# Optimization experiments

Measured on AMD Instinct MI355X. Metric: run time of the kernel, lower is better.

The kernel has to match this reference:

```python
import jax, jax.numpy as jnp
import numpy as np

B, C, HH, WW = 4, 128, 64, 64
NH = 2                      # n_heads
D = C // NH                 # head dim
N = HH * WW                 # tokens


def setup_inputs() -> dict:
    key = jax.random.key(0)
    ks = jax.random.split(key, 8)
    s = 1.0 / np.sqrt(C)
    return {
        "x": jax.random.normal(ks[0], (B, C, HH, WW), dtype=jnp.float32),
        "wq": jax.random.normal(ks[1], (C, C), dtype=jnp.float32) * s,
        "bq": jnp.zeros((C,), dtype=jnp.float32),
        "wk": jax.random.normal(ks[2], (C, C), dtype=jnp.float32) * s,
        "bk": jnp.zeros((C,), dtype=jnp.float32),
        "wv": jax.random.normal(ks[3], (C, C), dtype=jnp.float32) * s,
        "bv": jnp.zeros((C,), dtype=jnp.float32),
        "pe": jax.random.normal(ks[4], (N, D, NH), dtype=jnp.float32),
    }


def reference(x, wq, bq, wk, bk, wv, bv, pe):
    b, c, h, w = x.shape
    nh = pe.shape[2]
    d = c // nh
    n = h * w
    xf = x.reshape(b, c, n)                       # flatten spatial -> tokens
    # 1x1 convs == per-pixel channel matmuls
    q = jnp.einsum('oc,bcn->bon', wq, xf) + bq[None, :, None]
    k = jnp.einsum('oc,bcn->bon', wk, xf) + bk[None, :, None]
    v = jnp.einsum('oc,bcn->bon', wv, xf) + bv[None, :, None]
    q = q.reshape(b, nh, d, n)
    k = k.reshape(b, nh, d, n)
    v = v.reshape(b, nh, d, n)
    # learned positional encoding added to q: pe [n, d, nh] -> [nh, d, n]
    q = q + jnp.transpose(pe, (2, 1, 0))[None]
    scale = jnp.asarray(c, x.dtype) ** -0.25
    scores = jnp.einsum('bhdn,bhdm->bhnm', q, k) * scale   # [b,nh,n,n]
    attn = jax.nn.softmax(scores, axis=-1)
    # dropout is identity in eval mode
    o = jnp.einsum('bhnm,bhdm->bhdn', attn, v)             # [b,nh,d,n]
    attn_out = jnp.transpose(o.reshape(b, nh, d, h, w), (0, 2, 1, 3, 4))
    out = attn_out.reshape(b, c, h, w)
    return (out, attn_out)
```

## Files before the change

kernel.cpp:

```cpp
#include <hip/hip_runtime.h>
#include <hip/hip_bf16.h>

typedef unsigned short ushort_t;
typedef unsigned int   uint_t;
typedef unsigned short ushortx8 __attribute__((ext_vector_type(8)));
typedef unsigned short ushortx4 __attribute__((ext_vector_type(4)));
typedef unsigned int   uintx4   __attribute__((ext_vector_type(4)));
typedef __bf16        bf16x8   __attribute__((ext_vector_type(8)));
typedef float         f32x4    __attribute__((ext_vector_type(4)));
typedef float         f32x16   __attribute__((ext_vector_type(16)));

#define SCALE_QL (0.29730177875068026f * 1.4426950408889634f)
#define OUT_HALF 2097152
#define NSPLIT   4
#define KT_SPLIT 16
#define MFIX     32.0f

static __device__ __forceinline__ float fexp2(float x) {
    float r; asm("v_exp_f32 %0, %1" : "=v"(r) : "v"(x)); return r;
}
static __device__ __forceinline__ unsigned cvtpk_bf16(float lo, float hi) {
    unsigned r;
    asm("v_cvt_pk_bf16_f32 %0, %1, %2" : "=v"(r) : "v"(lo), "v"(hi));
    return r;
}
static __device__ __forceinline__ void pswap(unsigned& a, unsigned& b) {
    asm("v_permlane32_swap_b32 %0, %1" : "+v"(a), "+v"(b));
}
static __device__ __forceinline__ ushort_t bf16u(float f) {
    __hip_bfloat16 h = __float2bfloat16(f);
    return __builtin_bit_cast(ushort_t, h);
}
static __device__ __forceinline__ float bflo(unsigned u) {
    return __builtin_bit_cast(float, u << 16);
}
static __device__ __forceinline__ float bfhi(unsigned u) {
    return __builtin_bit_cast(float, u & 0xffff0000u);
}
static __device__ __forceinline__ void glds16(const void* g, void* l) {
    __builtin_amdgcn_global_load_lds(
        (const __attribute__((address_space(1))) unsigned int*)g,
        (__attribute__((address_space(3))) unsigned int*)l, 16, 0, 0);
}

__global__ __launch_bounds__(256) void prep_kernel(
    const float* __restrict__ pe,
    const float* __restrict__ wq, const float* __restrict__ wk,
    const float* __restrict__ wv,
    float* __restrict__ pet, ushort_t* __restrict__ wb)
{
    const int bid = blockIdx.x, t = threadIdx.x;
    if (bid < 1024) {
        int idx = bid * 256 + t;
        float2 p2 = *(const float2*)(pe + (size_t)idx * 2);
        pet[idx]                     = p2.x;
        pet[(size_t)4096 * 64 + idx] = p2.y;
        return;
    }
    const int b2 = bid - 1024;
    const int p  = b2 >> 3;
    const float* w = (p == 0) ? wq : (p == 1) ? wk : wv;
    const int cid = (b2 & 7) * 256 + t;
    const int o = cid >> 4, chunk = cid & 15;
    float4 f0 = *(const float4*)(w + o * 128 + chunk * 8);
    float4 f1 = *(const float4*)(w + o * 128 + chunk * 8 + 4);
    ushortx8 u;
    u[0] = bf16u(f0.x); u[1] = bf16u(f0.y); u[2] = bf16u(f0.z); u[3] = bf16u(f0.w);
    u[4] = bf16u(f1.x); u[5] = bf16u(f1.y); u[6] = bf16u(f1.z); u[7] = bf16u(f1.w);
    *(ushortx8*)(wb + p * 16384 + o * 128 + ((chunk ^ (o & 15)) << 3)) = u;
}

__global__ __launch_bounds__(256, 2) void proj_kernel(
    const float* __restrict__ x, const ushort_t* __restrict__ wb,
    const float* __restrict__ bq, const float* __restrict__ bk,
    const float* __restrict__ bv, const float* __restrict__ pet,
    ushort_t* __restrict__ qw, ushort_t* __restrict__ kw,
    ushort_t* __restrict__ vw)
{
    const int ntl = blockIdx.x;
    const int b = blockIdx.y;
    __shared__ __align__(16) ushort_t xt[64 * 128];
    __shared__ __align__(16) union {
        ushort_t xs[128][68];
        ushort_t wt[16384];
    } smu;
    const int t = threadIdx.x, lane = t & 63;
    const int wv_ = __builtin_amdgcn_readfirstlane(t >> 6);
    const int l16 = lane & 15, lhi = lane >> 4;

    {
        const int cg = t >> 4, n0 = (t & 15) * 4;
#pragma unroll
        for (int i = 0; i < 8; ++i) {
            int c = i * 16 + cg;
            float4 f = *(const float4*)(x + ((size_t)(b * 128 + c)) * 4096 + ntl * 64 + n0);
            ushortx4 u;
            u[0] = bf16u(f.x); u[1] = bf16u(f.y); u[2] = bf16u(f.z); u[3] = bf16u(f.w);
            *(ushortx4*)(&smu.xs[c][n0]) = u;
        }
    }
    __syncthreads();
    {
        const int n = t >> 2;
#pragma unroll
        for (int j = 0; j < 4; ++j) {
            int chunk = (t & 3) * 4 + j;
            ushortx8 u;
#pragma unroll
            for (int e = 0; e < 8; ++e) u[e] = smu.xs[chunk * 8 + e][n];
            *(ushortx8*)(xt + n * 128 + ((chunk ^ (n & 15)) << 3)) = u;
        }
    }

    const int nbase = ntl * 64;
    const char* xbp = (const char*)xt;
    const char* wbp = (const char*)smu.wt;

    for (int p = 0; p < 3; ++p) {
        __syncthreads();
        const ushort_t* wsrc = wb + p * 16384;
#pragma unroll
        for (int j = 0; j < 8; ++j) {
            int row = wv_ * 32 + j * 4;
            glds16(wsrc + row * 128 + lane * 8, smu.wt + row * 128);
        }

        const float* bias = (p == 0) ? bq : (p == 1) ? bk : bv;
        f32x4 bias4[2];
        bias4[0] = *(const f32x4*)(bias + wv_ * 32 + lhi * 4);
        bias4[1] = *(const f32x4*)(bias + wv_ * 32 + 16 + lhi * 4);
        f32x4 acc[2][4];
#pragma unroll
        for (int mf = 0; mf < 2; ++mf)
#pragma unroll
            for (int nf = 0; nf < 4; ++nf) acc[mf][nf] = bias4[mf];

        __syncthreads();

#pragma unroll
        for (int ks = 0; ks < 4; ++ks) {
            bf16x8 af[2];
#pragma unroll
            for (int mf = 0; mf < 2; ++mf) {
                int row = wv_ * 32 + mf * 16 + l16;
                af[mf] = __builtin_bit_cast(bf16x8, *(const ushortx8*)(
                    wbp + row * 256 + ((((ks * 4 + lhi) ^ l16) & 15) << 4)));
            }
#pragma unroll
            for (int nf = 0; nf < 4; ++nf) {
                int row = nf * 16 + l16;
                bf16x8 bfr = __builtin_bit_cast(bf16x8, *(const ushortx8*)(
                    xbp + row * 256 + ((((ks * 4 + lhi) ^ l16) & 15) << 4)));
                acc[0][nf] = __builtin_amdgcn_mfma_f32_16x16x32_bf16(af[0], bfr, acc[0][nf], 0, 0, 0);
                acc[1][nf] = __builtin_amdgcn_mfma_f32_16x16x32_bf16(af[1], bfr, acc[1][nf], 0, 0, 0);
            }
        }

        if (p == 2) {
#pragma unroll
            for (int mf = 0; mf < 2; ++mf) {
                int o = wv_ * 32 + mf * 16 + lhi * 4;
                int h = o >> 6, d = o & 63;
                ushort_t* vb = vw + (((size_t)(b * 2 + h) * 64 + d)) * 4096 + nbase + l16;
#pragma unroll
                for (int nf = 0; nf < 4; ++nf)
#pragma unroll
                    for (int r = 0; r < 4; ++r)
                        vb[(size_t)r * 4096 + nf * 16] = bf16u(acc[mf][nf][r]);
            }
        } else if (p == 0) {
#pragma unroll
            for (int mf = 0; mf < 2; ++mf) {
                int o = wv_ * 32 + mf * 16 + lhi * 4;
                int h = o >> 6, d = o & 63;
#pragma unroll
                for (int nf = 0; nf < 4; ++nf) {
                    int n = nbase + nf * 16 + l16;
                    f32x4 pe4 = *(const f32x4*)(pet + ((size_t)h * 4096 + n) * 64 + d);
                    f32x4 q4 = (acc[mf][nf] + pe4) * SCALE_QL;
                    ushortx4 s;
                    s[0] = bf16u(q4[0]); s[1] = bf16u(q4[1]);
                    s[2] = bf16u(q4[2]); s[3] = bf16u(q4[3]);
                    *(ushortx4*)(qw + ((size_t)(b * 2 + h) * 4096 + n) * 64 + d) = s;
                }
            }
        } else {
#pragma unroll
            for (int mf = 0; mf < 2; ++mf) {
                int o = wv_ * 32 + mf * 16 + lhi * 4;
                int h = o >> 6, d = o & 63;
#pragma unroll
                for (int nf = 0; nf < 4; ++nf) {
                    int n = nbase + nf * 16 + l16;
                    f32x4 k4 = acc[mf][nf];
                    ushortx4 s;
                    s[0] = bf16u(k4[0]); s[1] = bf16u(k4[1]);
                    s[2] = bf16u(k4[2]); s[3] = bf16u(k4[3]);
                    *(ushortx4*)(kw + ((size_t)(b * 2 + h) * 4096 + n) * 64 + d) = s;
                }
            }
        }
    }
}

__global__ __launch_bounds__(512, 4) void attn_kernel(
    const ushort_t* __restrict__ qw, const ushort_t* __restrict__ kw,
    const ushort_t* __restrict__ vw, uint_t* __restrict__ opart,
    float* __restrict__ lspart)
{
    const int qt = blockIdx.x, bh = blockIdx.y, sp = blockIdx.z;
    const int t = threadIdx.x, lane = t & 63;
    const int wv = t >> 6;
    const int l31 = lane & 31, hi = lane >> 5;

    __shared__ __align__(16) ushort_t Kt[2 * 64 * 64];
    __shared__ __align__(16) ushort_t Vt[2 * 64 * 64];

    const int qb = qt * 256 + wv * 32;
    bf16x8 qf[4];
#pragma unroll
    for (int ks = 0; ks < 4; ++ks)
        qf[ks] = __builtin_bit_cast(bf16x8, *(const ushortx8*)(
            qw + ((size_t)bh * 4096 + qb + l31) * 64 + ks * 16 + hi * 8));

    const ushort_t* kgb = kw + ((size_t)bh * 4096) * 64;
    const ushort_t* vgb = vw + ((size_t)bh * 64) * 4096;

    const int srow = lane >> 3, c7 = lane & 7;
    const int rb = wv * 8;
    const int swz = (c7 ^ srow) << 3;
    const size_t koff = (size_t)(rb + srow) * 64 + swz;
    const size_t voff = (size_t)(rb + srow) * 4096 + swz;

    const f32x16 z16 = {0,0,0,0,0,0,0,0,0,0,0,0,0,0,0,0};
    f32x16 oa0 = z16, oa1 = z16;
    float ls0 = 0.f;

    const int kt0 = sp * KT_SPLIT;

#define STAGE(buf, ktb)                                                       \
    {                                                                         \
        glds16(kgb + (size_t)(ktb) * 4096 + koff,                             \
               Kt + (buf) * 4096 + (size_t)rb * 64);                          \
        glds16(vgb + (size_t)(ktb) * 64 + voff,                               \
               Vt + (buf) * 4096 + (size_t)rb * 64);                          \
    }

    STAGE(0, kt0)
    __syncthreads();

    const int sw7 = l31 & 7;
    int cur = 0;
    for (int it = 0; it < KT_SPLIT; ++it) {
        const int itn = (it + 1 < KT_SPLIT) ? it + 1 : it;
        STAGE(cur ^ 1, kt0 + itn)

        const char* kc = (const char*)(Kt + cur * 4096);
        const char* vc = (const char*)(Vt + cur * 4096);

#pragma unroll
        for (int c = 0; c < 2; ++c) {
            const int kbase = (c * 32 + l31) * 128;
            bf16x8 kf[4];
#pragma unroll
            for (int ks = 0; ks < 4; ++ks)
                kf[ks] = __builtin_bit_cast(bf16x8, *(const ushortx8*)(
                    kc + kbase + (((ks * 2 + hi) ^ sw7) << 4)));

            f32x16 s0 = z16;
            __builtin_amdgcn_s_setprio(1);
#pragma unroll
            for (int ks = 0; ks < 4; ++ks)
                s0 = __builtin_amdgcn_mfma_f32_32x32x16_bf16(kf[ks], qf[ks], s0, 0, 0, 0);
            __builtin_amdgcn_s_setprio(0);

            float p[16];
#pragma unroll
            for (int r = 0; r < 16; ++r) p[r] = fexp2(s0[r] - MFIX);
            float q0 = (p[0] + p[1]) + (p[2] + p[3]);
            float q1 = (p[4] + p[5]) + (p[6] + p[7]);
            float q2 = (p[8] + p[9]) + (p[10] + p[11]);
            float q3 = (p[12] + p[13]) + (p[14] + p[15]);
            ls0 += (q0 + q1) + (q2 + q3);
            unsigned c0 = cvtpk_bf16(p[0], p[1]);
            unsigned c1 = cvtpk_bf16(p[2], p[3]);
            unsigned c2 = cvtpk_bf16(p[4], p[5]);
            unsigned c3 = cvtpk_bf16(p[6], p[7]);
            unsigned c4 = cvtpk_bf16(p[8], p[9]);
            unsigned c5 = cvtpk_bf16(p[10], p[11]);
            unsigned c6 = cvtpk_bf16(p[12], p[13]);
            unsigned c7x = cvtpk_bf16(p[14], p[15]);
            pswap(c0, c2); pswap(c1, c3); pswap(c4, c6); pswap(c5, c7x);
            bf16x8 pfa, pfb;
            { uintx4 u; u[0] = c0; u[1] = c1; u[2] = c2; u[3] = c3;
              pfa = __builtin_bit_cast(bf16x8, u); }
            { uintx4 u; u[0] = c4; u[1] = c5; u[2] = c6; u[3] = c7x;
              pfb = __builtin_bit_cast(bf16x8, u); }

            __builtin_amdgcn_s_setprio(1);
            {
                const int vb0 = l31 * 128;
                bf16x8 vf0 = __builtin_bit_cast(bf16x8, *(const ushortx8*)(
                    vc + vb0 + ((((c * 2 + 0) * 2 + hi) ^ sw7) << 4)));
                bf16x8 vf1 = __builtin_bit_cast(bf16x8, *(const ushortx8*)(
                    vc + vb0 + ((((c * 2 + 1) * 2 + hi) ^ sw7) << 4)));
                oa0 = __builtin_amdgcn_mfma_f32_32x32x16_bf16(vf0, pfa, oa0, 0, 0, 0);
                oa0 = __builtin_amdgcn_mfma_f32_32x32x16_bf16(vf1, pfb, oa0, 0, 0, 0);
            }
            {
                const int vb1 = (32 + l31) * 128;
                bf16x8 vf0 = __builtin_bit_cast(bf16x8, *(const ushortx8*)(
                    vc + vb1 + ((((c * 2 + 0) * 2 + hi) ^ sw7) << 4)));
                bf16x8 vf1 = __builtin_bit_cast(bf16x8, *(const ushortx8*)(
                    vc + vb1 + ((((c * 2 + 1) * 2 + hi) ^ sw7) << 4)));
                oa1 = __builtin_amdgcn_mfma_f32_32x32x16_bf16(vf0, pfa, oa1, 0, 0, 0);
                oa1 = __builtin_amdgcn_mfma_f32_32x32x16_bf16(vf1, pfb, oa1, 0, 0, 0);
            }
            __builtin_amdgcn_s_setprio(0);
        }

        __syncthreads();
        cur ^= 1;
    }

    const int pidx = (qt * 8 + bh) * NSPLIT + sp;
#define STORE_OA(OA, DT)                                                      \
    {                                                                         \
        uintx4 u0, u1;                                                        \
        u0[0] = cvtpk_bf16(OA[0], OA[1]);  u0[1] = cvtpk_bf16(OA[2], OA[3]);  \
        u0[2] = cvtpk_bf16(OA[4], OA[5]);  u0[3] = cvtpk_bf16(OA[6], OA[7]);  \
        u1[0] = cvtpk_bf16(OA[8], OA[9]);  u1[1] = cvtpk_bf16(OA[10], OA[11]);\
        u1[2] = cvtpk_bf16(OA[12], OA[13]);u1[3] = cvtpk_bf16(OA[14], OA[15]);\
        uint_t* dst = opart +                                                 \
            (((size_t)pidx * 8 + wv) * 2 + (DT)) * 512 + lane * 8;            \
        *(uintx4*)dst = u0; *(uintx4*)(dst + 4) = u1;                         \
    }
    STORE_OA(oa0, 0) STORE_OA(oa1, 1)

    ls0 += __shfl_xor(ls0, 32, 64);
    if (hi == 0)
        lspart[(pidx * 8 + wv) * 32 + l31] = ls0;
}

__global__ __launch_bounds__(512) void combine_kernel(
    const uint_t* __restrict__ opart, const float* __restrict__ lspart,
    float* __restrict__ out)
{
    const int qt = blockIdx.x, bh = blockIdx.y;
    const int b = bh >> 1, h = bh & 1;
    const int t = threadIdx.x, lane = t & 63, wa = t >> 6;
    const int l31 = lane & 31, hi = lane >> 5;
    const int pbase = (qt * 8 + bh) * NSPLIT;
    const int dtbl[8] = {0, 2, 8, 10, 16, 18, 24, 26};

    float den = 0.f;
#pragma unroll
    for (int sp = 0; sp < NSPLIT; ++sp)
        den += lspart[((pbase + sp) * 8 + wa) * 32 + l31];
    float inv = 1.f / den;

    const int q = qt * 256 + wa * 32 + l31;
#pragma unroll
    for (int dt = 0; dt < 2; ++dt) {
        float acc[16];
#pragma unroll
        for (int i = 0; i < 16; ++i) acc[i] = 0.f;
#pragma unroll
        for (int sp = 0; sp < NSPLIT; ++sp) {
            const uint_t* src = opart +
                (((size_t)(pbase + sp) * 8 + wa) * 2 + dt) * 512 + lane * 8;
            uintx4 a = *(const uintx4*)src;
            uintx4 b2 = *(const uintx4*)(src + 4);
#pragma unroll
            for (int j = 0; j < 4; ++j) {
                acc[2 * j]     += bflo(a[j]);
                acc[2 * j + 1] += bfhi(a[j]);
                acc[8 + 2 * j] += bflo(b2[j]);
                acc[9 + 2 * j] += bfhi(b2[j]);
            }
        }
#pragma unroll
        for (int j = 0; j < 8; ++j) {
            int d = dt * 32 + 4 * hi + dtbl[j];
            float v0 = acc[2 * j] * inv;
            float v1 = acc[2 * j + 1] * inv;
            size_t o0 = ((size_t)(b * 128 + d * 2 + h)) * 4096 + q;
            out[o0] = v0;
            out[o0 + OUT_HALF] = v0;
            size_t o1 = o0 + 2 * 4096;
            out[o1] = v1;
            out[o1 + OUT_HALF] = v1;
        }
    }
}

extern "C" void kernel_launch(void* const* d_in, const int* in_sizes, int n_in,
                              void* d_out, int out_size, void* d_ws, size_t ws_size,
                              hipStream_t stream) {
    const float* x  = (const float*)d_in[0];
    const float* wq = (const float*)d_in[1];
    const float* bq = (const float*)d_in[2];
    const float* wk = (const float*)d_in[3];
    const float* bk = (const float*)d_in[4];
    const float* wv = (const float*)d_in[5];
    const float* bv = (const float*)d_in[6];
    const float* pe = (const float*)d_in[7];
    float* out = (float*)d_out;

    char* ws = (char*)d_ws;
    float*    pet   = (float*)ws;
    ushort_t* qw    = (ushort_t*)(ws + (size_t)2  * 1024 * 1024);
    ushort_t* kw    = (ushort_t*)(ws + (size_t)6  * 1024 * 1024);
    ushort_t* vw    = (ushort_t*)(ws + (size_t)10 * 1024 * 1024);
    uint_t*   opart = (uint_t*)(ws + (size_t)14 * 1024 * 1024);
    float*    lsprt = (float*)(ws + (size_t)31 * 1024 * 1024);
    ushort_t* wb    = (ushort_t*)(ws + (size_t)31 * 1024 * 1024);

    hipLaunchKernelGGL(prep_kernel, dim3(1048), dim3(256), 0, stream,
                       pe, wq, wk, wv, pet, wb);
    hipLaunchKernelGGL(proj_kernel, dim3(64, 4), dim3(256), 0, stream,
                       x, wb, bq, bk, bv, pet, qw, kw, vw);
    hipLaunchKernelGGL(attn_kernel, dim3(16, 8, NSPLIT), dim3(512), 0, stream,
                       qw, kw, vw, opart, lsprt);
    hipLaunchKernelGGL(combine_kernel, dim3(16, 8), dim3(512), 0, stream,
                       opart, lsprt, out);
}
```

Baseline: 70.53 us.

## Split projection across grid z and double attention K/V tile size

The projection kernel now launches one block per (tile, batch, projection) instead of looping over Q/K/V in one block. This triples the block count to improve occupancy, but each block reloads and converts the x tile. The attention kernel stages 128-key tiles instead of 64 and halves the per-split iteration count, which cuts barriers and loop overhead per key. In exchange it doubles LDS use for the K/V double buffers, which may reduce how many blocks fit on a CU.

```diff
diff --git a/kernel.cpp b/kernel.cpp
--- a/kernel.cpp
+++ b/kernel.cpp
@@ -13,7 +13,7 @@
 #define SCALE_QL (0.29730177875068026f * 1.4426950408889634f)
 #define OUT_HALF 2097152
 #define NSPLIT   4
-#define KT_SPLIT 16
+#define KT_SPLIT 8
 #define MFIX     32.0f
 
 static __device__ __forceinline__ float fexp2(float x) {
@@ -78,7 +78,7 @@
     ushort_t* __restrict__ vw)
 {
     const int ntl = blockIdx.x;
-    const int b = blockIdx.y;
+    const int b = blockIdx.y, p = blockIdx.z;
     __shared__ __align__(16) ushort_t xt[64 * 128];
     __shared__ __align__(16) union {
         ushort_t xs[128][68];
@@ -111,93 +111,92 @@
             *(ushortx8*)(xt + n * 128 + ((chunk ^ (n & 15)) << 3)) = u;
         }
     }
+    __syncthreads();
+
+    {
+        const ushort_t* wsrc = wb + p * 16384;
+#pragma unroll
+        for (int j = 0; j < 8; ++j) {
+            int row = wv_ * 32 + j * 4;
+            glds16(wsrc + row * 128 + lane * 8, smu.wt + row * 128);
+        }
+    }
+
+    const float* bias = (p == 0) ? bq : (p == 1) ? bk : bv;
+    f32x4 bias4[2];
+    bias4[0] = *(const f32x4*)(bias + wv_ * 32 + lhi * 4);
+    bias4[1] = *(const f32x4*)(bias + wv_ * 32 + 16 + lhi * 4);
+    f32x4 acc[2][4];
+#pragma unroll
+    for (int mf = 0; mf < 2; ++mf)
+#pragma unroll
+        for (int nf = 0; nf < 4; ++nf) acc[mf][nf] = bias4[mf];
+
+    __syncthreads();
 
     const int nbase = ntl * 64;
     const char* xbp = (const char*)xt;
     const char* wbp = (const char*)smu.wt;
-
-    for (int p = 0; p < 3; ++p) {
-        __syncthreads();
-        const ushort_t* wsrc = wb + p * 16384;
-#pragma unroll
-        for (int j = 0; j < 8; ++j) {
-            int row = wv_ * 32 + j * 4;
-            glds16(wsrc + row * 128 + lane * 8, smu.wt + row * 128);
-        }
-
-        const float* bias = (p == 0) ? bq : (p == 1) ? bk : bv;
-        f32x4 bias4[2];
-        bias4[0] = *(const f32x4*)(bias + wv_ * 32 + lhi * 4);
-        bias4[1] = *(const f32x4*)(bias + wv_ * 32 + 16 + lhi * 4);
-        f32x4 acc[2][4];
-#pragma unroll
-        for (int mf = 0; mf < 2; ++mf)
-#pragma unroll
-            for (int nf = 0; nf < 4; ++nf) acc[mf][nf] = bias4[mf];
-
-        __syncthreads();
-
-#pragma unroll
-        for (int ks = 0; ks < 4; ++ks) {
-            bf16x8 af[2];
-#pragma unroll
-            for (int mf = 0; mf < 2; ++mf) {
-                int row = wv_ * 32 + mf * 16 + l16;
-                af[mf] = __builtin_bit_cast(bf16x8, *(const ushortx8*)(
-                    wbp + row * 256 + ((((ks * 4 + lhi) ^ l16) & 15) << 4)));
+#pragma unroll
+    for (int ks = 0; ks < 4; ++ks) {
+        bf16x8 af[2];
+#pragma unroll
+        for (int mf = 0; mf < 2; ++mf) {
+            int row = wv_ * 32 + mf * 16 + l16;
+            af[mf] = __builtin_bit_cast(bf16x8, *(const ushortx8*)(
+                wbp + row * 256 + ((((ks * 4 + lhi) ^ l16) & 15) << 4)));
+        }
+#pragma unroll
+        for (int nf = 0; nf < 4; ++nf) {
+            int row = nf * 16 + l16;
+            bf16x8 bfr = __builtin_bit_cast(bf16x8, *(const ushortx8*)(
+                xbp + row * 256 + ((((ks * 4 + lhi) ^ l16) & 15) << 4)));
+            acc[0][nf] = __builtin_amdgcn_mfma_f32_16x16x32_bf16(af[0], bfr, acc[0][nf], 0, 0, 0);
+            acc[1][nf] = __builtin_amdgcn_mfma_f32_16x16x32_bf16(af[1], bfr, acc[1][nf], 0, 0, 0);
+        }
+    }
+
+    if (p == 2) {
+#pragma unroll
+        for (int mf = 0; mf < 2; ++mf) {
+            int o = wv_ * 32 + mf * 16 + lhi * 4;
+            int h = o >> 6, d = o & 63;
+            ushort_t* vb = vw + (((size_t)(b * 2 + h) * 64 + d)) * 4096 + nbase + l16;
+#pragma unroll
+            for (int nf = 0; nf < 4; ++nf)
+#pragma unroll
+                for (int r = 0; r < 4; ++r)
+                    vb[(size_t)r * 4096 + nf * 16] = bf16u(acc[mf][nf][r]);
+        }
+    } else if (p == 0) {
+#pragma unroll
+        for (int mf = 0; mf < 2; ++mf) {
+            int o = wv_ * 32 + mf * 16 + lhi * 4;
+            int h = o >> 6, d = o & 63;
+#pragma unroll
+            for (int nf = 0; nf < 4; ++nf) {
+                int n = nbase + nf * 16 + l16;
+                f32x4 pe4 = *(const f32x4*)(pet + ((size_t)h * 4096 + n) * 64 + d);
+                f32x4 q4 = (acc[mf][nf] + pe4) * SCALE_QL;
+                ushortx4 s;
+                s[0] = bf16u(q4[0]); s[1] = bf16u(q4[1]);
+                s[2] = bf16u(q4[2]); s[3] = bf16u(q4[3]);
+                *(ushortx4*)(qw + ((size_t)(b * 2 + h) * 4096 + n) * 64 + d) = s;
             }
+        }
+    } else {
+#pragma unroll
+        for (int mf = 0; mf < 2; ++mf) {
+            int o = wv_ * 32 + mf * 16 + lhi * 4;
+            int h = o >> 6, d = o & 63;
 #pragma unroll
             for (int nf = 0; nf < 4; ++nf) {
-                int row = nf * 16 + l16;
-                bf16x8 bfr = __builtin_bit_cast(bf16x8, *(const ushortx8*)(
-                    xbp + row * 256 + ((((ks * 4 + lhi) ^ l16) & 15) << 4)));
-                acc[0][nf] = __builtin_amdgcn_mfma_f32_16x16x32_bf16(af[0], bfr, acc[0][nf], 0, 0, 0);
-                acc[1][nf] = __builtin_amdgcn_mfma_f32_16x16x32_bf16(af[1], bfr, acc[1][nf], 0, 0, 0);
-            }
-        }
-
-        if (p == 2) {
-#pragma unroll
-            for (int mf = 0; mf < 2; ++mf) {
-                int o = wv_ * 32 + mf * 16 + lhi * 4;
-                int h = o >> 6, d = o & 63;
-                ushort_t* vb = vw + (((size_t)(b * 2 + h) * 64 + d)) * 4096 + nbase + l16;
-#pragma unroll
-                for (int nf = 0; nf < 4; ++nf)
-#pragma unroll
-                    for (int r = 0; r < 4; ++r)
-                        vb[(size_t)r * 4096 + nf * 16] = bf16u(acc[mf][nf][r]);
-            }
-        } else if (p == 0) {
-#pragma unroll
-            for (int mf = 0; mf < 2; ++mf) {
-                int o = wv_ * 32 + mf * 16 + lhi * 4;
-                int h = o >> 6, d = o & 63;
-#pragma unroll
-                for (int nf = 0; nf < 4; ++nf) {
-                    int n = nbase + nf * 16 + l16;
-                    f32x4 pe4 = *(const f32x4*)(pet + ((size_t)h * 4096 + n) * 64 + d);
-                    f32x4 q4 = (acc[mf][nf] + pe4) * SCALE_QL;
-                    ushortx4 s;
-                    s[0] = bf16u(q4[0]); s[1] = bf16u(q4[1]);
-                    s[2] = bf16u(q4[2]); s[3] = bf16u(q4[3]);
-                    *(ushortx4*)(qw + ((size_t)(b * 2 + h) * 4096 + n) * 64 + d) = s;
-                }
-            }
-        } else {
-#pragma unroll
-            for (int mf = 0; mf < 2; ++mf) {
-                int o = wv_ * 32 + mf * 16 + lhi * 4;
-                int h = o >> 6, d = o & 63;
-#pragma unroll
-                for (int nf = 0; nf < 4; ++nf) {
-                    int n = nbase + nf * 16 + l16;
-                    f32x4 k4 = acc[mf][nf];
-                    ushortx4 s;
-                    s[0] = bf16u(k4[0]); s[1] = bf16u(k4[1]);
-                    s[2] = bf16u(k4[2]); s[3] = bf16u(k4[3]);
-                    *(ushortx4*)(kw + ((size_t)(b * 2 + h) * 4096 + n) * 64 + d) = s;
-                }
+                int n = nbase + nf * 16 + l16;
+                f32x4 k4 = acc[mf][nf];
+                ushortx4 s;
+                s[0] = bf16u(k4[0]); s[1] = bf16u(k4[1]);
+                s[2] = bf16u(k4[2]); s[3] = bf16u(k4[3]);
+                *(ushortx4*)(kw + ((size_t)(b * 2 + h) * 4096 + n) * 64 + d) = s;
             }
         }
     }
@@ -213,8 +212,8 @@
     const int wv = t >> 6;
     const int l31 = lane & 31, hi = lane >> 5;
 
-    __shared__ __align__(16) ushort_t Kt[2 * 64 * 64];
-    __shared__ __align__(16) ushort_t Vt[2 * 64 * 64];
+    __shared__ __align__(16) ushort_t Kt[2 * 8192];
+    __shared__ __align__(16) ushort_t Vt[2 * 8192];
 
     const int qb = qt * 256 + wv * 32;
     bf16x8 qf[4];
@@ -227,10 +226,10 @@
     const ushort_t* vgb = vw + ((size_t)bh * 64) * 4096;
 
     const int srow = lane >> 3, c7 = lane & 7;
-    const int rb = wv * 8;
     const int swz = (c7 ^ srow) << 3;
-    const size_t koff = (size_t)(rb + srow) * 64 + swz;
-    const size_t voff = (size_t)(rb + srow) * 4096 + swz;
+    const size_t kofa = (size_t)(wv * 16 + srow) * 64 + swz;
+    const size_t kofb = (size_t)(wv * 16 + 8 + srow) * 64 + swz;
+    const size_t vofa = (size_t)(wv * 8 + srow) * 4096 + swz;
 
     const f32x16 z16 = {0,0,0,0,0,0,0,0,0,0,0,0,0,0,0,0};
     f32x16 oa0 = z16, oa1 = z16;
@@ -240,10 +239,14 @@
 
 #define STAGE(buf, ktb)                                                       \
     {                                                                         \
-        glds16(kgb + (size_t)(ktb) * 4096 + koff,                             \
-               Kt + (buf) * 4096 + (size_t)rb * 64);                          \
-        glds16(vgb + (size_t)(ktb) * 64 + voff,                               \
-               Vt + (buf) * 4096 + (size_t)rb * 64);                          \
+        const ushort_t* kg = kgb + (size_t)(ktb) * 8192;                      \
+        const ushort_t* vg = vgb + (size_t)(ktb) * 128;                       \
+        ushort_t* kd = Kt + (buf) * 8192;                                     \
+        ushort_t* vd = Vt + (buf) * 8192;                                     \
+        glds16(kg + kofa, kd + (size_t)(wv * 16) * 64);                       \
+        glds16(kg + kofb, kd + (size_t)(wv * 16 + 8) * 64);                   \
+        glds16(vg + vofa,      vd + wv * 512);                                \
+        glds16(vg + 64 + vofa, vd + 4096 + wv * 512);                         \
     }
 
     STAGE(0, kt0)
@@ -255,11 +258,11 @@
         const int itn = (it + 1 < KT_SPLIT) ? it + 1 : it;
         STAGE(cur ^ 1, kt0 + itn)
 
-        const char* kc = (const char*)(Kt + cur * 4096);
-        const char* vc = (const char*)(Vt + cur * 4096);
-
-#pragma unroll
-        for (int c = 0; c < 2; ++c) {
+        const char* kc  = (const char*)Kt + cur * 16384;
+        const char* vcb = (const char*)Vt + cur * 16384;
+
+#pragma unroll
+        for (int c = 0; c < 4; ++c) {
             const int kbase = (c * 32 + l31) * 128;
             bf16x8 kf[4];
 #pragma unroll
@@ -297,22 +300,24 @@
             { uintx4 u; u[0] = c4; u[1] = c5; u[2] = c6; u[3] = c7x;
               pfb = __builtin_bit_cast(bf16x8, u); }
 
+            const char* vs = vcb + (c >> 1) * 8192;
+            const int cc = c & 1;
             __builtin_amdgcn_s_setprio(1);
             {
                 const int vb0 = l31 * 128;
                 bf16x8 vf0 = __builtin_bit_cast(bf16x8, *(const ushortx8*)(
-                    vc + vb0 + ((((c * 2 + 0) * 2 + hi) ^ sw7) << 4)));
+                    vs + vb0 + ((((cc * 2 + 0) * 2 + hi) ^ sw7) << 4)));
                 bf16x8 vf1 = __builtin_bit_cast(bf16x8, *(const ushortx8*)(
-                    vc + vb0 + ((((c * 2 + 1) * 2 + hi) ^ sw7) << 4)));
+                    vs + vb0 + ((((cc * 2 + 1) * 2 + hi) ^ sw7) << 4)));
                 oa0 = __builtin_amdgcn_mfma_f32_32x32x16_bf16(vf0, pfa, oa0, 0, 0, 0);
                 oa0 = __builtin_amdgcn_mfma_f32_32x32x16_bf16(vf1, pfb, oa0, 0, 0, 0);
             }
             {
                 const int vb1 = (32 + l31) * 128;
                 bf16x8 vf0 = __builtin_bit_cast(bf16x8, *(const ushortx8*)(
-                    vc + vb1 + ((((c * 2 + 0) * 2 + hi) ^ sw7) << 4)));
+                    vs + vb1 + ((((cc * 2 + 0) * 2 + hi) ^ sw7) << 4)));
                 bf16x8 vf1 = __builtin_bit_cast(bf16x8, *(const ushortx8*)(
-                    vc + vb1 + ((((c * 2 + 1) * 2 + hi) ^ sw7) << 4)));
+                    vs + vb1 + ((((cc * 2 + 1) * 2 + hi) ^ sw7) << 4)));
                 oa1 = __builtin_amdgcn_mfma_f32_32x32x16_bf16(vf0, pfa, oa1, 0, 0, 0);
                 oa1 = __builtin_amdgcn_mfma_f32_32x32x16_bf16(vf1, pfb, oa1, 0, 0, 0);
             }
@@ -418,7 +423,7 @@
 
     hipLaunchKernelGGL(prep_kernel, dim3(1048), dim3(256), 0, stream,
                        pe, wq, wk, wv, pet, wb);
-    hipLaunchKernelGGL(proj_kernel, dim3(64, 4), dim3(256), 0, stream,
+    hipLaunchKernelGGL(proj_kernel, dim3(64, 4, 3), dim3(256), 0, stream,
                        x, wb, bq, bk, bv, pet, qw, kw, vw);
     hipLaunchKernelGGL(attn_kernel, dim3(16, 8, NSPLIT), dim3(512), 0, stream,
                        qw, kw, vw, opart, lsprt);
```

Result: no change. 71.03 us (+0.7%).
